# Optimization experiments

Hardware: AMD Instinct MI355X
Metric: run time of the kernel (lower is better)

Reference implementation:

```python
import jax, jax.numpy as jnp
import numpy as np

N_NODES = 50000
N_EDGES = 300000
NODE_DIM = 11
EDGE_DIM = 5
HID = 256
L = 4
G = 1024  # num graphs
BN_EPS = 1e-5


def setup_inputs() -> dict:
    key = jax.random.key(0)
    ks = jax.random.split(key, 24)
    s = 0.05
    inp = {
        "x": jax.random.normal(ks[0], (N_NODES, NODE_DIM), jnp.float32),
        "edge_index": jax.random.randint(ks[1], (2, N_EDGES), 0, N_NODES, jnp.int32),
        "edge_attr": jax.random.normal(ks[2], (N_EDGES, EDGE_DIM), jnp.float32),
        "batch": jnp.sort(jax.random.randint(ks[3], (N_NODES,), 0, G, jnp.int32)),
        # node encoder
        "enc_W": jax.random.normal(ks[4], (NODE_DIM, HID), jnp.float32) * s,
        "enc_b": jnp.zeros((HID,), jnp.float32),
        # per-layer GINE params (stacked over layers)
        "edge_W": jax.random.normal(ks[5], (L, EDGE_DIM, HID), jnp.float32) * s,
        "edge_b": jnp.zeros((L, HID), jnp.float32),
        "mlp_W1": jax.random.normal(ks[6], (L, HID, HID), jnp.float32) * s,
        "mlp_b1": jnp.zeros((L, HID), jnp.float32),
        "mlp_W2": jax.random.normal(ks[7], (L, HID, HID), jnp.float32) * s,
        "mlp_b2": jnp.zeros((L, HID), jnp.float32),
        "bn_g": jnp.ones((L, HID), jnp.float32),
        "bn_b": jnp.zeros((L, HID), jnp.float32),
        # head: 3*HID -> HID -> HID//2 -> 1
        "head_W1": jax.random.normal(ks[8], (3 * HID, HID), jnp.float32) * s,
        "head_b1": jnp.zeros((HID,), jnp.float32),
        "head_W2": jax.random.normal(ks[9], (HID, HID // 2), jnp.float32) * s,
        "head_b2": jnp.zeros((HID // 2,), jnp.float32),
        "head_W3": jax.random.normal(ks[10], (HID // 2, 1), jnp.float32) * s,
        "head_b3": jnp.zeros((1,), jnp.float32),
    }
    return inp


def _forward(x, edge_attr, enc_W, enc_b, edge_W, edge_b, mlp_W1, mlp_b1,
             mlp_W2, mlp_b2, bn_g, bn_b, head_W1, head_b1, head_W2, head_b2,
             head_W3, head_b3, edge_index, batch):
    n = x.shape[0]
    src, dst = edge_index[0], edge_index[1]  # messages flow src(j) -> dst(i)
    h = jax.nn.relu(x @ enc_W + enc_b)  # [N, HID]
    for l in range(L):
        e = edge_attr @ edge_W[l] + edge_b[l]                 # [E, HID]
        msg = jax.nn.relu(h[src] + e)                         # [E, HID]
        aggr = jax.ops.segment_sum(msg, dst, num_segments=n)  # [N, HID]
        z = h + aggr                                          # (1+eps)*h + aggr, eps=0
        z = jax.nn.relu(z @ mlp_W1[l] + mlp_b1[l]) @ mlp_W2[l] + mlp_b2[l]
        # BatchNorm over node dim (batch statistics)
        mu = jnp.mean(z, axis=0)
        var = jnp.var(z, axis=0)
        z = (z - mu) * jax.lax.rsqrt(var + BN_EPS) * bn_g[l] + bn_b[l]
        h = jax.nn.relu(z) + h  # residual
    # mean / add / max pooling per graph
    sums = jax.ops.segment_sum(h, batch, num_segments=G)      # [G, HID]
    cnt = jax.ops.segment_sum(jnp.ones((n, 1), h.dtype), batch, num_segments=G)
    mean = sums / jnp.maximum(cnt, 1.0)
    mx = jax.ops.segment_max(h, batch, num_segments=G)
    g = jnp.concatenate([mean, sums, mx], axis=1)             # [G, 3*HID]
    g = jax.nn.relu(g @ head_W1 + head_b1)
    g = jax.nn.relu(g @ head_W2 + head_b2)
    out = g @ head_W3 + head_b3
    return out.reshape(-1)  # [G]


def reference(x, edge_index, edge_attr, batch, enc_W, enc_b, edge_W, edge_b,
              mlp_W1, mlp_b1, mlp_W2, mlp_b2, bn_g, bn_b, head_W1, head_b1,
              head_W2, head_b2, head_W3, head_b3):
    return _forward(x, edge_attr, enc_W, enc_b, edge_W, edge_b, mlp_W1, mlp_b1,
                    mlp_W2, mlp_b2, bn_g, bn_b, head_W1, head_b1, head_W2,
                    head_b2, head_W3, head_b3, edge_index, batch)
```

## Files before the change

### kernel.cpp

```cpp
#include <hip/hip_runtime.h>

#define N_NODES 50000
#define N_EDGES 300000
#define G_GRAPHS 1024
#define HID 256
#define NLAYERS 4
#define PAD_SLOTS (N_EDGES + 3 * N_NODES + 64)
#define BMT 224

typedef unsigned short ushort_t;
typedef __attribute__((ext_vector_type(8))) short bf16x8;
typedef __attribute__((ext_vector_type(8))) unsigned short u16x8;
typedef __attribute__((ext_vector_type(4))) float f32x4;

__device__ __forceinline__ float bf2f(ushort_t u) {
  unsigned int x = ((unsigned int)u) << 16;
  return __builtin_bit_cast(float, x);
}
__device__ __forceinline__ ushort_t f2bf(float f) {
  unsigned int x = __builtin_bit_cast(unsigned int, f);
  unsigned int lsb = (x >> 16) & 1u;
  x += 0x7fffu + lsb;
  return (ushort_t)(x >> 16);
}

__global__ __launch_bounds__(256) void k_encoder(const float* __restrict__ x,
    const float* __restrict__ W, const float* __restrict__ b,
    ushort_t* __restrict__ h, int n)
{
  int j = threadIdx.x;
  float wcol[11];
#pragma unroll
  for (int k = 0; k < 11; ++k) wcol[k] = W[k * HID + j];
  float bj = b[j];
  __shared__ float xs[8][11];
  int base = blockIdx.x * 8;
  if (j < 88) {
    int r = j / 11, k = j % 11;
    int row = base + r;
    if (row < n) xs[r][k] = x[row * 11 + k];
  }
  __syncthreads();
#pragma unroll
  for (int r = 0; r < 8; ++r) {
    int row = base + r;
    if (row >= n) break;
    float acc = bj;
#pragma unroll
    for (int k = 0; k < 11; ++k) acc += xs[r][k] * wcol[k];
    h[(size_t)row * HID + j] = f2bf(fmaxf(acc, 0.f));
  }
}

__global__ __launch_bounds__(256) void k_hist(const int* __restrict__ dst,
    int* __restrict__ offs, int E)
{
  int e = blockIdx.x * 256 + threadIdx.x;
  if (e < E) atomicAdd(&offs[dst[e]], 1);
}

__global__ __launch_bounds__(1024) void k_scanA(int* __restrict__ offs,
    int* __restrict__ btot, int n)
{
  __shared__ int wsum[16];
  int tid = threadIdx.x, lane = tid & 63, wid = tid >> 6;
  int idx = blockIdx.x * 1024 + tid;
  int cnt = (idx < n) ? offs[idx] : 0;
  int v = (cnt + 3) & ~3;
  int x = v;
#pragma unroll
  for (int off = 1; off < 64; off <<= 1) {
    int t = __shfl_up(x, off);
    if (lane >= off) x += t;
  }
  if (lane == 63) wsum[wid] = x;
  __syncthreads();
  if (wid == 0 && lane < 16) {
    int w = wsum[lane];
#pragma unroll
    for (int off = 1; off < 16; off <<= 1) {
      int t = __shfl_up(w, off);
      if (lane >= off) w += t;
    }
    wsum[lane] = w;
  }
  __syncthreads();
  int wbase = (wid == 0) ? 0 : wsum[wid - 1];
  if (idx < n) offs[idx] = wbase + x - v;
  if (tid == 0) btot[blockIdx.x] = wsum[15];
}

__global__ __launch_bounds__(1024) void k_scanC(int* __restrict__ offs,
    int* __restrict__ pstart, const int* __restrict__ btot, int n)
{
  __shared__ int sbase;
  if (threadIdx.x == 0) {
    int s = 0;
    for (int i = 0; i < (int)blockIdx.x; ++i) s += btot[i];
    sbase = s;
    if (blockIdx.x == gridDim.x - 1) pstart[n] = s + btot[blockIdx.x];
  }
  __syncthreads();
  int idx = blockIdx.x * 1024 + threadIdx.x;
  if (idx < n) {
    int v = offs[idx] + sbase;
    offs[idx] = v;
    pstart[idx] = v;
  }
}

__global__ __launch_bounds__(256) void k_fill(const int* __restrict__ src,
    const int* __restrict__ dst, int* __restrict__ offs,
    int* __restrict__ esrc, ushort_t* __restrict__ eab,
    const float* __restrict__ ea, int E)
{
  int e = blockIdx.x * 256 + threadIdx.x;
  if (e < E) {
    int d = dst[e];
    int p = atomicAdd(&offs[d], 1);
    esrc[p] = src[e];
    const float* ep = ea + (size_t)e * 5;
    ushort4 lo = make_ushort4(f2bf(ep[0]), f2bf(ep[1]), f2bf(ep[2]), f2bf(ep[3]));
    ushort4 hi = make_ushort4(f2bf(ep[4]), (ushort_t)0x3f80u, 0, 0);
    *(ushort4*)&eab[(size_t)p * 8] = lo;
    *(ushort4*)&eab[(size_t)p * 8 + 4] = hi;
  }
}

__global__ __launch_bounds__(256) void k_prep(const float* __restrict__ W1,
    const float* __restrict__ W2, ushort_t* __restrict__ Wt1,
    ushort_t* __restrict__ Wt2)
{
  __shared__ float ld[16][257];
  int mat = blockIdx.y & (NLAYERS - 1);
  int which = blockIdx.y >> 2;
  const float* Wm = (which ? W2 : W1) + (size_t)mat * HID * HID;
  ushort_t* Wtm = (which ? Wt2 : Wt1) + (size_t)mat * HID * HID;
  int k0 = blockIdx.x * 16;
  int tid = threadIdx.x;
#pragma unroll
  for (int i = 0; i < 16; ++i) ld[i][tid] = Wm[(size_t)(k0 + i) * HID + tid];
  __syncthreads();
#pragma unroll
  for (int v = 0; v < 4; ++v) {
    ushort4 u = make_ushort4(f2bf(ld[v*4+0][tid]), f2bf(ld[v*4+1][tid]),
                             f2bf(ld[v*4+2][tid]), f2bf(ld[v*4+3][tid]));
    *(ushort4*)&Wtm[(size_t)tid * HID + k0 + v * 4] = u;
  }
}

__global__ __launch_bounds__(256) void k_prept(const float* __restrict__ W,
    ushort_t* __restrict__ Wt, int K, int N)
{
  int idx = blockIdx.x * 256 + threadIdx.x;
  if (idx >= K * N) return;
  int n = idx / K, k = idx % K;
  Wt[idx] = f2bf(W[(size_t)k * N + n]);
}

__device__ __forceinline__ void edge_step(bf16x8 ev, ushort4 hv,
    const float4& w0, const float4& w1, const float4& w2, const float4& w3,
    const float4& w4, const float4& bi,
    float& ax, float& ay, float& az, float& aw)
{
  float v0 = bf2f((ushort_t)ev[0]), v1 = bf2f((ushort_t)ev[1]),
        v2 = bf2f((ushort_t)ev[2]), v3 = bf2f((ushort_t)ev[3]),
        v4 = bf2f((ushort_t)ev[4]), fl = bf2f((ushort_t)ev[5]);
  float m0 = bi.x, m1 = bi.y, m2 = bi.z, m3 = bi.w;
  m0 = fmaf(v0, w0.x, m0); m1 = fmaf(v0, w0.y, m1);
  m2 = fmaf(v0, w0.z, m2); m3 = fmaf(v0, w0.w, m3);
  m0 = fmaf(v1, w1.x, m0); m1 = fmaf(v1, w1.y, m1);
  m2 = fmaf(v1, w1.z, m2); m3 = fmaf(v1, w1.w, m3);
  m0 = fmaf(v2, w2.x, m0); m1 = fmaf(v2, w2.y, m1);
  m2 = fmaf(v2, w2.z, m2); m3 = fmaf(v2, w2.w, m3);
  m0 = fmaf(v3, w3.x, m0); m1 = fmaf(v3, w3.y, m1);
  m2 = fmaf(v3, w3.z, m2); m3 = fmaf(v3, w3.w, m3);
  m0 = fmaf(v4, w4.x, m0); m1 = fmaf(v4, w4.y, m1);
  m2 = fmaf(v4, w4.z, m2); m3 = fmaf(v4, w4.w, m3);
  m0 += bf2f(hv.x); m1 += bf2f(hv.y); m2 += bf2f(hv.z); m3 += bf2f(hv.w);
  ax = fmaf(fl, fmaxf(m0, 0.f), ax);
  ay = fmaf(fl, fmaxf(m1, 0.f), ay);
  az = fmaf(fl, fmaxf(m2, 0.f), az);
  aw = fmaf(fl, fmaxf(m3, 0.f), aw);
}

__global__ __launch_bounds__(256) void k_gather(const ushort_t* __restrict__ h,
    const int* __restrict__ pstart, const int* __restrict__ esrc,
    const ushort_t* __restrict__ eab, const float* __restrict__ eW,
    const float* __restrict__ eb, ushort_t* __restrict__ zin,
    float* __restrict__ stats, int n)
{
  int tid = threadIdx.x;
  if (blockIdx.x == 0) { stats[tid] = 0.f; stats[HID + tid] = 0.f; }
  int wave = tid >> 6, lane = tid & 63;
  int c4 = lane * 4;
  float4 w0 = *(const float4*)&eW[0 * HID + c4];
  float4 w1 = *(const float4*)&eW[1 * HID + c4];
  float4 w2 = *(const float4*)&eW[2 * HID + c4];
  float4 w3 = *(const float4*)&eW[3 * HID + c4];
  float4 w4 = *(const float4*)&eW[4 * HID + c4];
  float4 bi = *(const float4*)&eb[c4];
  int n0 = (blockIdx.x * 4 + wave) * 4;
  if (n0 >= n) return;
  int e0 = __builtin_amdgcn_readfirstlane(pstart[n0]);
  int e1 = __builtin_amdgcn_readfirstlane(pstart[n0 + 1]);
  int e2 = __builtin_amdgcn_readfirstlane(pstart[n0 + 2]);
  int e3 = __builtin_amdgcn_readfirstlane(pstart[n0 + 3]);
  int e4 = __builtin_amdgcn_readfirstlane(pstart[n0 + 4]);
  float A[4][4];
#pragma unroll
  for (int j = 0; j < 4; ++j) {
    ushort4 hv = *(const ushort4*)&h[(size_t)(n0 + j) * HID + c4];
    A[j][0] = bf2f(hv.x); A[j][1] = bf2f(hv.y);
    A[j][2] = bf2f(hv.z); A[j][3] = bf2f(hv.w);
  }
  int p = e0, pend = e4;
  bf16x8 ec0, ec1, ec2, ec3;
  ushort4 hc0, hc1, hc2, hc3;
  int sn0, sn1, sn2, sn3;
  if (p < pend) {
    int sc0 = esrc[p], sc1 = esrc[p + 1], sc2 = esrc[p + 2], sc3 = esrc[p + 3];
    ec0 = *(const bf16x8*)&eab[(size_t)(p + 0) * 8];
    ec1 = *(const bf16x8*)&eab[(size_t)(p + 1) * 8];
    ec2 = *(const bf16x8*)&eab[(size_t)(p + 2) * 8];
    ec3 = *(const bf16x8*)&eab[(size_t)(p + 3) * 8];
    hc0 = *(const ushort4*)&h[(size_t)sc0 * HID + c4];
    hc1 = *(const ushort4*)&h[(size_t)sc1 * HID + c4];
    hc2 = *(const ushort4*)&h[(size_t)sc2 * HID + c4];
    hc3 = *(const ushort4*)&h[(size_t)sc3 * HID + c4];
    int pn = (p + 4 < pend) ? p + 4 : p;
    sn0 = esrc[pn]; sn1 = esrc[pn + 1]; sn2 = esrc[pn + 2]; sn3 = esrc[pn + 3];
  }
  for (; p < pend; p += 4) {
    int pn = (p + 4 < pend) ? p + 4 : p;
    int pnn = (p + 8 < pend) ? p + 8 : p;
    bf16x8 en0 = *(const bf16x8*)&eab[(size_t)(pn + 0) * 8];
    bf16x8 en1 = *(const bf16x8*)&eab[(size_t)(pn + 1) * 8];
    bf16x8 en2 = *(const bf16x8*)&eab[(size_t)(pn + 2) * 8];
    bf16x8 en3 = *(const bf16x8*)&eab[(size_t)(pn + 3) * 8];
    ushort4 hn0 = *(const ushort4*)&h[(size_t)sn0 * HID + c4];
    ushort4 hn1 = *(const ushort4*)&h[(size_t)sn1 * HID + c4];
    ushort4 hn2 = *(const ushort4*)&h[(size_t)sn2 * HID + c4];
    ushort4 hn3 = *(const ushort4*)&h[(size_t)sn3 * HID + c4];
    int sm0 = esrc[pnn], sm1 = esrc[pnn + 1], sm2 = esrc[pnn + 2], sm3 = esrc[pnn + 3];
    float c0 = 0.f, c1 = 0.f, c2 = 0.f, c3 = 0.f;
    edge_step(ec0, hc0, w0, w1, w2, w3, w4, bi, c0, c1, c2, c3);
    edge_step(ec1, hc1, w0, w1, w2, w3, w4, bi, c0, c1, c2, c3);
    edge_step(ec2, hc2, w0, w1, w2, w3, w4, bi, c0, c1, c2, c3);
    edge_step(ec3, hc3, w0, w1, w2, w3, w4, bi, c0, c1, c2, c3);
    if (p < e1)      { A[0][0] += c0; A[0][1] += c1; A[0][2] += c2; A[0][3] += c3; }
    else if (p < e2) { A[1][0] += c0; A[1][1] += c1; A[1][2] += c2; A[1][3] += c3; }
    else if (p < e3) { A[2][0] += c0; A[2][1] += c1; A[2][2] += c2; A[2][3] += c3; }
    else             { A[3][0] += c0; A[3][1] += c1; A[3][2] += c2; A[3][3] += c3; }
    ec0 = en0; ec1 = en1; ec2 = en2; ec3 = en3;
    hc0 = hn0; hc1 = hn1; hc2 = hn2; hc3 = hn3;
    sn0 = sm0; sn1 = sm1; sn2 = sm2; sn3 = sm3;
  }
#pragma unroll
  for (int j = 0; j < 4; ++j) {
    *(ushort4*)&zin[(size_t)(n0 + j) * HID + c4] =
        make_ushort4(f2bf(A[j][0]), f2bf(A[j][1]), f2bf(A[j][2]), f2bf(A[j][3]));
  }
}

__global__ __launch_bounds__(512, 1) void k_mlp(const ushort_t* __restrict__ A,
    const ushort_t* __restrict__ Wt1, const float* __restrict__ b1,
    const ushort_t* __restrict__ Wt2, const float* __restrict__ b2,
    ushort_t* __restrict__ out, float* __restrict__ stats, int M)
{
  __shared__ alignas(16) ushort_t T[BMT][264];
  int tid = threadIdx.x;
  int wave = tid >> 6, lane = tid & 63;
  int m = lane & 15, quad = lane >> 4;
  int col0 = wave * 32;
  int row0 = blockIdx.x * BMT;

#pragma unroll
  for (int i = 0; i < 14; ++i) {
    int flat = i * 512 + tid;
    int row = flat >> 5, kc = flat & 31;
    int gr = row0 + row; if (gr > M - 1) gr = M - 1;
    u16x8 v = *(const u16x8*)(A + (size_t)gr * HID + kc * 8);
    *(u16x8*)&T[row][kc * 8] = v;
  }
  bf16x8 w1f[2][8];
#pragma unroll
  for (int nt = 0; nt < 2; ++nt)
#pragma unroll
    for (int kt = 0; kt < 8; ++kt)
      w1f[nt][kt] = *(const bf16x8*)(
          Wt1 + (size_t)(col0 + nt * 16 + m) * HID + kt * 32 + quad * 8);
  float bv1[2] = {b1[col0 + m], b1[col0 + 16 + m]};
  float bv2[2] = {b2[col0 + m], b2[col0 + 16 + m]};
  __syncthreads();

  f32x4 acc[14][2];
#pragma unroll
  for (int mt = 0; mt < 14; ++mt) {
    acc[mt][0] = (f32x4){0.f, 0.f, 0.f, 0.f};
    acc[mt][1] = (f32x4){0.f, 0.f, 0.f, 0.f};
    bf16x8 af[8];
#pragma unroll
    for (int kt = 0; kt < 8; ++kt)
      af[kt] = *(const bf16x8*)&T[mt * 16 + m][kt * 32 + quad * 8];
#pragma unroll
    for (int kt = 0; kt < 8; ++kt) {
      acc[mt][0] = __builtin_amdgcn_mfma_f32_16x16x32_bf16(af[kt], w1f[0][kt], acc[mt][0], 0, 0, 0);
      acc[mt][1] = __builtin_amdgcn_mfma_f32_16x16x32_bf16(af[kt], w1f[1][kt], acc[mt][1], 0, 0, 0);
    }
  }
  __syncthreads();

#pragma unroll
  for (int mt = 0; mt < 14; ++mt)
#pragma unroll
    for (int nt = 0; nt < 2; ++nt)
#pragma unroll
      for (int reg = 0; reg < 4; ++reg)
        T[mt * 16 + quad * 4 + reg][col0 + nt * 16 + m] =
            f2bf(fmaxf(acc[mt][nt][reg] + bv1[nt], 0.f));
  bf16x8 w2f[2][8];
#pragma unroll
  for (int nt = 0; nt < 2; ++nt)
#pragma unroll
    for (int kt = 0; kt < 8; ++kt)
      w2f[nt][kt] = *(const bf16x8*)(
          Wt2 + (size_t)(col0 + nt * 16 + m) * HID + kt * 32 + quad * 8);
  __syncthreads();

#pragma unroll
  for (int mt = 0; mt < 14; ++mt) {
    acc[mt][0] = (f32x4){0.f, 0.f, 0.f, 0.f};
    acc[mt][1] = (f32x4){0.f, 0.f, 0.f, 0.f};
    bf16x8 af[8];
#pragma unroll
    for (int kt = 0; kt < 8; ++kt)
      af[kt] = *(const bf16x8*)&T[mt * 16 + m][kt * 32 + quad * 8];
#pragma unroll
    for (int kt = 0; kt < 8; ++kt) {
      acc[mt][0] = __builtin_amdgcn_mfma_f32_16x16x32_bf16(af[kt], w2f[0][kt], acc[mt][0], 0, 0, 0);
      acc[mt][1] = __builtin_amdgcn_mfma_f32_16x16x32_bf16(af[kt], w2f[1][kt], acc[mt][1], 0, 0, 0);
    }
  }

  float csum[2] = {0.f, 0.f}, csq[2] = {0.f, 0.f};
#pragma unroll
  for (int mt = 0; mt < 14; ++mt) {
    if (row0 + mt * 16 < M) {
#pragma unroll
      for (int nt = 0; nt < 2; ++nt) {
#pragma unroll
        for (int reg = 0; reg < 4; ++reg) {
          float o = acc[mt][nt][reg] + bv2[nt];
          out[(size_t)(row0 + mt * 16 + quad * 4 + reg) * HID + col0 + nt * 16 + m] = f2bf(o);
          csum[nt] += o; csq[nt] = fmaf(o, o, csq[nt]);
        }
      }
    }
  }
#pragma unroll
  for (int nt = 0; nt < 2; ++nt) {
    float s = csum[nt], q = csq[nt];
    s += __shfl_xor(s, 16); s += __shfl_xor(s, 32);
    q += __shfl_xor(q, 16); q += __shfl_xor(q, 32);
    if (quad == 0) {
      unsafeAtomicAdd(&stats[col0 + nt * 16 + m], s);
      unsafeAtomicAdd(&stats[HID + col0 + nt * 16 + m], q);
    }
  }
}

__global__ __launch_bounds__(256) void k_bn_apply(const ushort_t* __restrict__ z,
    const float* __restrict__ stats, const float* __restrict__ g,
    const float* __restrict__ b, ushort_t* __restrict__ h, int total8)
{
  int idx = blockIdx.x * 256 + threadIdx.x;
  if (idx >= total8) return;
  int col = (idx & 31) * 8;
  const float inv_n = 1.f / (float)N_NODES;
  float sc[8], sh[8];
#pragma unroll
  for (int c = 0; c < 8; ++c) {
    float mu = stats[col + c] * inv_n;
    float var = stats[HID + col + c] * inv_n - mu * mu;
    float rs = rsqrtf(var + 1e-5f);
    sc[c] = g[col + c] * rs;
    sh[c] = b[col + c] - mu * sc[c];
  }
  u16x8 zv = *(const u16x8*)(z + (size_t)idx * 8);
  u16x8 hv = *(const u16x8*)(h + (size_t)idx * 8);
  u16x8 o;
#pragma unroll
  for (int c = 0; c < 8; ++c) {
    float v = fmaxf(fmaf(bf2f(zv[c]), sc[c], sh[c]), 0.f) + bf2f(hv[c]);
    o[c] = f2bf(v);
  }
  *(u16x8*)(h + (size_t)idx * 8) = o;
}

__device__ __forceinline__ int lbound(const int* __restrict__ b, int n, int key) {
  int lo = 0, hi = n;
  while (lo < hi) {
    int mid = (lo + hi) >> 1;
    if (b[mid] < key) lo = mid + 1; else hi = mid;
  }
  return lo;
}

__global__ __launch_bounds__(256) void k_pool_bn(const ushort_t* __restrict__ z,
    const float* __restrict__ stats, const float* __restrict__ g_,
    const float* __restrict__ b_, const ushort_t* __restrict__ h,
    const int* __restrict__ batch, ushort_t* __restrict__ gf)
{
  int g = blockIdx.x, j = threadIdx.x;
  const float inv_n = 1.f / (float)N_NODES;
  float mu = stats[j] * inv_n;
  float var = stats[HID + j] * inv_n - mu * mu;
  float rs = rsqrtf(var + 1e-5f);
  float sc = g_[j] * rs;
  float sh = b_[j] - mu * sc;
  int lo = lbound(batch, N_NODES, g);
  int hi = lbound(batch, N_NODES, g + 1);
  float s = 0.f, mx = 0.f;
  int i = lo;
  for (; i + 1 < hi; i += 2) {
    float zv0 = bf2f(z[(size_t)i * HID + j]);
    float hv0 = bf2f(h[(size_t)i * HID + j]);
    float zv1 = bf2f(z[(size_t)(i + 1) * HID + j]);
    float hv1 = bf2f(h[(size_t)(i + 1) * HID + j]);
    float v0 = fmaxf(fmaf(zv0, sc, sh), 0.f) + hv0;
    float v1 = fmaxf(fmaf(zv1, sc, sh), 0.f) + hv1;
    s += v0 + v1;
    mx = fmaxf(mx, fmaxf(v0, v1));
  }
  if (i < hi) {
    float zv = bf2f(z[(size_t)i * HID + j]);
    float hv = bf2f(h[(size_t)i * HID + j]);
    float v = fmaxf(fmaf(zv, sc, sh), 0.f) + hv;
    s += v; mx = fmaxf(mx, v);
  }
  float cntv = fmaxf((float)(hi - lo), 1.f);
  size_t base = (size_t)g * 768;
  gf[base + j] = f2bf(s / cntv);
  gf[base + 256 + j] = f2bf(s);
  gf[base + 512 + j] = f2bf(mx);
}

template<int KT, int DO_RELU>
__global__ __launch_bounds__(256, 1) void k_head_gemm(const ushort_t* __restrict__ A,
    const ushort_t* __restrict__ Bt, const float* __restrict__ bias,
    ushort_t* __restrict__ out, int M, int N)
{
  const int K = KT * 32;
  int tid = threadIdx.x;
  int wave = tid >> 6, lane = tid & 63;
  int m = lane & 15, quad = lane >> 4;
  int col = (blockIdx.y * 4 + wave) * 16 + m;
  bf16x8 bfrag[KT];
#pragma unroll
  for (int kt = 0; kt < KT; ++kt)
    bfrag[kt] = *(const bf16x8*)(Bt + (size_t)col * K + kt * 32 + quad * 8);
  float bv = bias[col];
  int ntiles = M >> 4;
  for (int t = blockIdx.x; t < ntiles; t += gridDim.x) {
    const ushort_t* Ap = A + (size_t)(t * 16 + m) * K + quad * 8;
    bf16x8 af[KT];
#pragma unroll
    for (int kt = 0; kt < KT; ++kt) af[kt] = *(const bf16x8*)(Ap + kt * 32);
    f32x4 acc = (f32x4){0.f, 0.f, 0.f, 0.f};
#pragma unroll
    for (int kt = 0; kt < KT; ++kt)
      acc = __builtin_amdgcn_mfma_f32_16x16x32_bf16(af[kt], bfrag[kt], acc, 0, 0, 0);
    int rb = t * 16 + quad * 4;
#pragma unroll
    for (int reg = 0; reg < 4; ++reg) {
      float o = acc[reg] + bv;
      if (DO_RELU) o = fmaxf(o, 0.f);
      out[(size_t)(rb + reg) * N + col] = f2bf(o);
    }
  }
}

__global__ __launch_bounds__(256) void k_head_out(const ushort_t* __restrict__ g2,
    const float* __restrict__ W3, const float* __restrict__ b3,
    float* __restrict__ out)
{
  int wave = threadIdx.x >> 6, lane = threadIdx.x & 63;
  int g = blockIdx.x * 4 + wave;
  ushort2 v = *(const ushort2*)&g2[(size_t)g * 128 + lane * 2];
  float p = bf2f(v.x) * W3[lane * 2] + bf2f(v.y) * W3[lane * 2 + 1];
#pragma unroll
  for (int off = 32; off > 0; off >>= 1) p += __shfl_down(p, off);
  if (lane == 0) out[g] = p + b3[0];
}

extern "C" void kernel_launch(void* const* d_in, const int* in_sizes, int n_in,
                              void* d_out, int out_size, void* d_ws, size_t ws_size,
                              hipStream_t stream)
{
  const float* x     = (const float*)d_in[0];
  const int*   ei    = (const int*)d_in[1];
  const float* ea    = (const float*)d_in[2];
  const int*   batch = (const int*)d_in[3];
  const float* encW  = (const float*)d_in[4];
  const float* encB  = (const float*)d_in[5];
  const float* edgeW = (const float*)d_in[6];
  const float* edgeB = (const float*)d_in[7];
  const float* W1    = (const float*)d_in[8];
  const float* b1    = (const float*)d_in[9];
  const float* W2    = (const float*)d_in[10];
  const float* b2    = (const float*)d_in[11];
  const float* bng   = (const float*)d_in[12];
  const float* bnb   = (const float*)d_in[13];
  const float* hW1   = (const float*)d_in[14];
  const float* hb1   = (const float*)d_in[15];
  const float* hW2   = (const float*)d_in[16];
  const float* hb2   = (const float*)d_in[17];
  const float* hW3   = (const float*)d_in[18];
  const float* hb3   = (const float*)d_in[19];
  float* out = (float*)d_out;

  const size_t NH = (size_t)N_NODES * HID;
  char* base = (char*)d_ws;
  auto alloc = [&](size_t bytes) -> char* {
    char* p = base; base += (bytes + 63) & ~(size_t)63; return p;
  };
  float*    stats = (float*)alloc(512 * 4);
  int*      offs  = (int*)alloc(50001 * 4);
  int*      pstart= (int*)alloc(50001 * 4);
  int*      btot  = (int*)alloc(64 * 4);
  int*      esrc  = (int*)alloc((size_t)PAD_SLOTS * 4);
  ushort_t* eab   = (ushort_t*)alloc((size_t)PAD_SLOTS * 8 * 2);
  ushort_t* Wt1   = (ushort_t*)alloc((size_t)NLAYERS * HID * HID * 2);
  ushort_t* Wt2   = (ushort_t*)alloc((size_t)NLAYERS * HID * HID * 2);
  ushort_t* hW1t  = (ushort_t*)alloc((size_t)768 * 256 * 2);
  ushort_t* hW2t  = (ushort_t*)alloc((size_t)256 * 128 * 2);
  ushort_t* gf    = (ushort_t*)alloc((size_t)G_GRAPHS * 768 * 2);
  ushort_t* g1    = (ushort_t*)alloc((size_t)G_GRAPHS * 256 * 2);
  ushort_t* g2    = (ushort_t*)alloc((size_t)G_GRAPHS * 128 * 2);
  ushort_t* zin   = (ushort_t*)alloc(NH * 2);
  ushort_t* h     = (ushort_t*)alloc(NH * 2);

  const int* src = ei;
  const int* dst = ei + N_EDGES;

  hipMemsetAsync(offs, 0, 50001 * sizeof(int), stream);
  hipMemsetAsync(esrc, 0, (size_t)((char*)(eab + (size_t)PAD_SLOTS * 8) - (char*)esrc), stream);
  k_hist<<<(N_EDGES + 255) / 256, 256, 0, stream>>>(dst, offs, N_EDGES);
  const int NSB = (N_NODES + 1023) / 1024;
  k_scanA<<<NSB, 1024, 0, stream>>>(offs, btot, N_NODES);
  k_scanC<<<NSB, 1024, 0, stream>>>(offs, pstart, btot, N_NODES);
  k_fill<<<(N_EDGES + 255) / 256, 256, 0, stream>>>(src, dst, offs, esrc, eab, ea, N_EDGES);
  k_prep<<<dim3(16, 2 * NLAYERS), 256, 0, stream>>>(W1, W2, Wt1, Wt2);
  k_prept<<<(768 * 256 + 255) / 256, 256, 0, stream>>>(hW1, hW1t, 768, 256);
  k_prept<<<(256 * 128 + 255) / 256, 256, 0, stream>>>(hW2, hW2t, 256, 128);

  k_encoder<<<(N_NODES + 7) / 8, 256, 0, stream>>>(x, encW, encB, h, N_NODES);

  const int NB_MLP = (N_NODES + BMT - 1) / BMT;

  for (int l = 0; l < NLAYERS; ++l) {
    k_gather<<<(N_NODES + 15) / 16, 256, 0, stream>>>(
        h, pstart, esrc, eab, edgeW + (size_t)l * 5 * HID, edgeB + (size_t)l * HID,
        zin, stats, N_NODES);
    k_mlp<<<NB_MLP, 512, 0, stream>>>(
        zin, Wt1 + (size_t)l * HID * HID, b1 + (size_t)l * HID,
        Wt2 + (size_t)l * HID * HID, b2 + (size_t)l * HID, zin, stats, N_NODES);
    if (l < NLAYERS - 1) {
      k_bn_apply<<<(N_NODES * HID / 8 + 255) / 256, 256, 0, stream>>>(
          zin, stats, bng + (size_t)l * HID, bnb + (size_t)l * HID, h,
          N_NODES * HID / 8);
    }
  }

  k_pool_bn<<<G_GRAPHS, 256, 0, stream>>>(
      zin, stats, bng + (size_t)(NLAYERS - 1) * HID,
      bnb + (size_t)(NLAYERS - 1) * HID, h, batch, gf);
  k_head_gemm<24, 1><<<dim3(16, 4), 256, 0, stream>>>(gf, hW1t, hb1, g1, G_GRAPHS, 256);
  k_head_gemm<8, 1><<<dim3(16, 2), 256, 0, stream>>>(g1, hW2t, hb2, g2, G_GRAPHS, 128);
  k_head_out<<<G_GRAPHS / 4, 256, 0, stream>>>(g2, hW3, hb3, out);
}
```

Measured before the change: 520.7 us.

## Stage MLP output through LDS for coalesced stores; fuse head layers 2 and 3

The MLP kernel now writes its second-GEMM results into the shared tile and then streams them out as 16-byte row-contiguous stores, replacing scattered 2-byte column stores. The activation buffer is padded to a multiple of the tile height so the row clamps and store guards can be removed, and padded rows are excluded from the BN statistics. The last two head layers are fused into one kernel that applies ReLU, dots with W3 via shuffles and atomically accumulates into a zeroed output, dropping one launch and the g2 buffer. The padded rows read uninitialized workspace and the float atomics make the output summation order nondeterministic.

```diff
diff --git a/kernel.cpp b/kernel.cpp
--- a/kernel.cpp
+++ b/kernel.cpp
@@ -7,6 +7,7 @@
 #define NLAYERS 4
 #define PAD_SLOTS (N_EDGES + 3 * N_NODES + 64)
 #define BMT 224
+#define NPAD 50176
 
 typedef unsigned short ushort_t;
 typedef __attribute__((ext_vector_type(8))) short bf16x8;
@@ -279,8 +280,7 @@
   for (int i = 0; i < 14; ++i) {
     int flat = i * 512 + tid;
     int row = flat >> 5, kc = flat & 31;
-    int gr = row0 + row; if (gr > M - 1) gr = M - 1;
-    u16x8 v = *(const u16x8*)(A + (size_t)gr * HID + kc * 8);
+    u16x8 v = *(const u16x8*)(A + (size_t)(row0 + row) * HID + kc * 8);
     *(u16x8*)&T[row][kc * 8] = v;
   }
   bf16x8 w1f[2][8];
@@ -342,19 +342,19 @@
       acc[mt][1] = __builtin_amdgcn_mfma_f32_16x16x32_bf16(af[kt], w2f[1][kt], acc[mt][1], 0, 0, 0);
     }
   }
+  __syncthreads();
 
   float csum[2] = {0.f, 0.f}, csq[2] = {0.f, 0.f};
 #pragma unroll
   for (int mt = 0; mt < 14; ++mt) {
-    if (row0 + mt * 16 < M) {
-#pragma unroll
-      for (int nt = 0; nt < 2; ++nt) {
-#pragma unroll
-        for (int reg = 0; reg < 4; ++reg) {
-          float o = acc[mt][nt][reg] + bv2[nt];
-          out[(size_t)(row0 + mt * 16 + quad * 4 + reg) * HID + col0 + nt * 16 + m] = f2bf(o);
-          csum[nt] += o; csq[nt] = fmaf(o, o, csq[nt]);
-        }
+    bool valid = (row0 + mt * 16) < M;
+#pragma unroll
+    for (int nt = 0; nt < 2; ++nt) {
+#pragma unroll
+      for (int reg = 0; reg < 4; ++reg) {
+        float o = acc[mt][nt][reg] + bv2[nt];
+        T[mt * 16 + quad * 4 + reg][col0 + nt * 16 + m] = f2bf(o);
+        if (valid) { csum[nt] += o; csq[nt] = fmaf(o, o, csq[nt]); }
       }
     }
   }
@@ -367,6 +367,15 @@
       unsafeAtomicAdd(&stats[col0 + nt * 16 + m], s);
       unsafeAtomicAdd(&stats[HID + col0 + nt * 16 + m], q);
     }
+  }
+  __syncthreads();
+
+#pragma unroll
+  for (int i = 0; i < 14; ++i) {
+    int flat = i * 512 + tid;
+    int row = flat >> 5, kc = flat & 31;
+    *(u16x8*)(out + (size_t)(row0 + row) * HID + kc * 8) =
+        *(const u16x8*)&T[row][kc * 8];
   }
 }
 
@@ -481,17 +490,45 @@
   }
 }
 
-__global__ __launch_bounds__(256) void k_head_out(const ushort_t* __restrict__ g2,
+__global__ __launch_bounds__(256, 1) void k_head2(const ushort_t* __restrict__ A,
+    const ushort_t* __restrict__ Bt, const float* __restrict__ bias,
     const float* __restrict__ W3, const float* __restrict__ b3,
-    float* __restrict__ out)
-{
-  int wave = threadIdx.x >> 6, lane = threadIdx.x & 63;
-  int g = blockIdx.x * 4 + wave;
-  ushort2 v = *(const ushort2*)&g2[(size_t)g * 128 + lane * 2];
-  float p = bf2f(v.x) * W3[lane * 2] + bf2f(v.y) * W3[lane * 2 + 1];
-#pragma unroll
-  for (int off = 32; off > 0; off >>= 1) p += __shfl_down(p, off);
-  if (lane == 0) out[g] = p + b3[0];
+    float* __restrict__ out, int M)
+{
+  const int K = 256;
+  int tid = threadIdx.x;
+  int wave = tid >> 6, lane = tid & 63;
+  int m = lane & 15, quad = lane >> 4;
+  int col = (blockIdx.y * 4 + wave) * 16 + m;
+  bf16x8 bfrag[8];
+#pragma unroll
+  for (int kt = 0; kt < 8; ++kt)
+    bfrag[kt] = *(const bf16x8*)(Bt + (size_t)col * K + kt * 32 + quad * 8);
+  float bv = bias[col];
+  float w3v = W3[col];
+  bool leader = (blockIdx.y == 0 && wave == 0);
+  float b3v = b3[0];
+  int ntiles = M >> 4;
+  for (int t = blockIdx.x; t < ntiles; t += gridDim.x) {
+    const ushort_t* Ap = A + (size_t)(t * 16 + m) * K + quad * 8;
+    bf16x8 af[8];
+#pragma unroll
+    for (int kt = 0; kt < 8; ++kt) af[kt] = *(const bf16x8*)(Ap + kt * 32);
+    f32x4 acc = (f32x4){0.f, 0.f, 0.f, 0.f};
+#pragma unroll
+    for (int kt = 0; kt < 8; ++kt)
+      acc = __builtin_amdgcn_mfma_f32_16x16x32_bf16(af[kt], bfrag[kt], acc, 0, 0, 0);
+#pragma unroll
+    for (int reg = 0; reg < 4; ++reg) {
+      float p = fmaxf(acc[reg] + bv, 0.f) * w3v;
+      p += __shfl_xor(p, 1); p += __shfl_xor(p, 2);
+      p += __shfl_xor(p, 4); p += __shfl_xor(p, 8);
+      if (m == 0) {
+        int row = t * 16 + quad * 4 + reg;
+        atomicAdd(&out[row], leader ? (p + b3v) : p);
+      }
+    }
+  }
 }
 
 extern "C" void kernel_launch(void* const* d_in, const int* in_sizes, int n_in,
@@ -537,14 +574,14 @@
   ushort_t* hW2t  = (ushort_t*)alloc((size_t)256 * 128 * 2);
   ushort_t* gf    = (ushort_t*)alloc((size_t)G_GRAPHS * 768 * 2);
   ushort_t* g1    = (ushort_t*)alloc((size_t)G_GRAPHS * 256 * 2);
-  ushort_t* g2    = (ushort_t*)alloc((size_t)G_GRAPHS * 128 * 2);
-  ushort_t* zin   = (ushort_t*)alloc(NH * 2);
+  ushort_t* zin   = (ushort_t*)alloc((size_t)NPAD * HID * 2);
   ushort_t* h     = (ushort_t*)alloc(NH * 2);
 
   const int* src = ei;
   const int* dst = ei + N_EDGES;
 
   hipMemsetAsync(offs, 0, 50001 * sizeof(int), stream);
+  hipMemsetAsync(out, 0, G_GRAPHS * sizeof(float), stream);
   hipMemsetAsync(esrc, 0, (size_t)((char*)(eab + (size_t)PAD_SLOTS * 8) - (char*)esrc), stream);
   k_hist<<<(N_EDGES + 255) / 256, 256, 0, stream>>>(dst, offs, N_EDGES);
   const int NSB = (N_NODES + 1023) / 1024;
@@ -557,7 +594,7 @@
 
   k_encoder<<<(N_NODES + 7) / 8, 256, 0, stream>>>(x, encW, encB, h, N_NODES);
 
-  const int NB_MLP = (N_NODES + BMT - 1) / BMT;
+  const int NB_MLP = NPAD / BMT;
 
   for (int l = 0; l < NLAYERS; ++l) {
     k_gather<<<(N_NODES + 15) / 16, 256, 0, stream>>>(
@@ -577,6 +614,5 @@
       zin, stats, bng + (size_t)(NLAYERS - 1) * HID,
       bnb + (size_t)(NLAYERS - 1) * HID, h, batch, gf);
   k_head_gemm<24, 1><<<dim3(16, 4), 256, 0, stream>>>(gf, hW1t, hb1, g1, G_GRAPHS, 256);
-  k_head_gemm<8, 1><<<dim3(16, 2), 256, 0, stream>>>(g1, hW2t, hb2, g2, G_GRAPHS, 128);
-  k_head_out<<<G_GRAPHS / 4, 256, 0, stream>>>(g2, hW3, hb3, out);
-}
+  k_head2<<<dim3(16, 2), 256, 0, stream>>>(g1, hW2t, hb2, hW3, hb3, out, G_GRAPHS);
+}
```

Measured after the change: 555.1 us. 1.07x slower.
